# Performance work log

Hardware: AMD Instinct MI355X
Metric: run time of the kernel (lower is better)

## Reference

```python
import jax, jax.numpy as jnp
import numpy as np

SEQ_LEN, USER_LEN = 20, 256
INPUT_SIZE = 100000
NUM_CENTROIDS = 64
CAND = 1024
HIDDEN_DIM = 128
TOPK = 10
RHO = 0.02


def setup_inputs() -> dict:
    key = jax.random.key(0)
    ks = jax.random.split(key, 20)
    s = 0.1  # modest weight scale
    return {
        "x": jax.random.randint(ks[0], (SEQ_LEN, USER_LEN), 0, INPUT_SIZE),
        "t_slot": jax.random.randint(ks[1], (SEQ_LEN, USER_LEN), 0, 168),
        "vecs_use": jax.random.normal(ks[2], (INPUT_SIZE, 20), jnp.float32),
        "x_embedding_network": jax.random.normal(ks[3], (INPUT_SIZE, HIDDEN_DIM), jnp.float32),
        "I_array": jax.random.randint(ks[4], (INPUT_SIZE,), 0, NUM_CENTROIDS),
        "cand": jax.random.randint(ks[5], (NUM_CENTROIDS, CAND), 0, INPUT_SIZE),
        "time_embeddings": jax.random.normal(ks[6], (4, 20), jnp.float32),
        "W_seq1": jax.random.normal(ks[7], (100, 40), jnp.float32) * s,
        "b_seq1": jnp.zeros((40,), jnp.float32),
        "W_seq2": jax.random.normal(ks[8], (40, 20), jnp.float32) * s,
        "b_seq2": jnp.zeros((20,), jnp.float32),
        "W_to1": jax.random.normal(ks[9], (40, 40), jnp.float32) * s,
        "b_to1": jnp.zeros((40,), jnp.float32),
        "W_to2": jax.random.normal(ks[10], (40, 20), jnp.float32) * s,
        "b_to2": jnp.zeros((20,), jnp.float32),
        "W_ti1": jax.random.normal(ks[11], (40, 40), jnp.float32) * s,
        "b_ti1": jnp.zeros((40,), jnp.float32),
        "W_ti2": jax.random.normal(ks[12], (40, 20), jnp.float32) * s,
        "b_ti2": jnp.zeros((20,), jnp.float32),
    }


def _map_hour_to_segment(t):
    h = t % 24
    return jnp.where((h >= 22) | (h < 6), 0, jnp.where(h < 14, 1, 2))


def reference(x, t_slot, vecs_use, x_embedding_network, I_array, cand,
              time_embeddings, W_seq1, b_seq1, W_seq2, b_seq2,
              W_to1, b_to1, W_to2, b_to2, W_ti1, b_ti1, W_ti2, b_ti2):
    seq_len, user_len = x.shape
    x_view = x.reshape(-1)                                  # [N]
    x_emb = vecs_use[x_view].reshape(seq_len, user_len, 20)  # [S,U,20]

    # time-transfer (outgoing): concat(loc_emb, time_emb[segment]) -> MLP
    seg = _map_hour_to_segment(t_slot.reshape(-1))
    xc = jnp.concatenate([x_emb.reshape(-1, 20), time_embeddings[seg]], axis=-1)
    xi_out = jax.nn.relu(xc @ W_to1 + b_to1) @ W_to2 + b_to2  # [N,20]

    # candidate side: every location paired with fixed target segment 2
    seg2 = jnp.broadcast_to(time_embeddings[2], (vecs_use.shape[0], 20))
    vo = jnp.concatenate([vecs_use, seg2], axis=-1)
    vec_output = jax.nn.relu(vo @ W_ti1 + b_ti1) @ W_ti2 + b_ti2  # [V,20]

    # 5-step history (shift-with-edge-repeat) concat -> seq MLP
    def shift(k):
        return jnp.concatenate([x_emb[:k], x_emb[:seq_len - k]], axis=0)
    hist = jnp.concatenate(
        [shift(4), shift(3), shift(2), shift(1), x_emb], axis=-1).reshape(-1, 100)
    hist = jax.nn.relu(hist @ W_seq1 + b_seq1) @ W_seq2 + b_seq2  # [N,20]

    # per-token cluster routing + candidate distances
    a = 0.5 * (hist + xi_out)            # [N,20]
    c_idx = I_array[x_view]              # [N] cluster of each token's location
    cand_tok = cand[c_idx]               # [N,C] candidate loc ids
    Vg = vec_output[cand_tok]            # [N,C,20]
    d2 = (jnp.sum(a * a, -1)[:, None] + jnp.sum(Vg * Vg, -1)
          - 2.0 * jnp.einsum('nd,ncd->nc', a, Vg))
    dist = jnp.sqrt(jnp.maximum(d2, 1e-12))
    score = jnp.exp(-RHO * dist)         # [N,C]

    values, idx = jax.lax.top_k(score, TOPK)                 # [N,K]
    neigh_ids = jnp.take_along_axis(cand_tok, idx, axis=1)   # [N,K]
    emb_neigh = x_embedding_network[neigh_ids]               # [N,K,H]
    self_emb = x_embedding_network[x_view][:, None, :]       # [N,1,H]
    emb_all = jnp.concatenate([emb_neigh, self_emb], axis=1)  # [N,K+1,H]
    vals = jnp.concatenate(
        [values, jnp.ones((values.shape[0], 1), values.dtype)], axis=-1)
    w = jax.nn.softmax(vals, axis=-1)                        # [N,K+1]
    return jnp.sum(emb_all * w[..., None], axis=1)           # [N,H]
```

## Files before the change

### kernel.cpp

```cpp
#include <hip/hip_runtime.h>
#include <hip/hip_bf16.h>

#define SEQ_LEN   20
#define USER_LEN  256
#define NTOK      (SEQ_LEN * USER_LEN)
#define NC        64
#define CAND_N    1024
#define HID       128
#define TOPK      10
#define RHO_C     0.02f

#define CAND_BLKS (NC * CAND_N / 32)
#define TOK_BLKS  (NTOK / 16)
#define MAXB      (NTOK / 8 + NC)

__global__ __launch_bounds__(256) void k_pre(
    const int* __restrict__ x, const int* __restrict__ t_slot,
    const float* __restrict__ vecs, const float* __restrict__ temb,
    const int* __restrict__ I_array, const int* __restrict__ cand,
    const float* __restrict__ Ws1, const float* __restrict__ bs1,
    const float* __restrict__ Ws2, const float* __restrict__ bs2,
    const float* __restrict__ Wt1, const float* __restrict__ bt1,
    const float* __restrict__ Wt2, const float* __restrict__ bt2,
    const float* __restrict__ Wc1, const float* __restrict__ bc1,
    const float* __restrict__ Wc2, const float* __restrict__ bc2,
    float* __restrict__ tab, float* __restrict__ aArr, float* __restrict__ aNorm,
    int* __restrict__ bucket, int* __restrict__ blkInfo) {
  __shared__ union {
    struct { float sIn[32][20]; float sHid[32][40]; float sOut[32][21]; float sT[20]; } cd;
    struct { float sIn[16][140]; float sHid[16][80]; } tk;
    struct { int lc[NC]; int lcur[NC]; } kb;
  } U;
  int tid = threadIdx.x;

  if (blockIdx.x < CAND_BLKS) {
    int cc = tid >> 3, t = tid & 7;
    int g = blockIdx.x * 32 + cc;
    int v = cand[g];
    if (tid < 20) U.cd.sT[tid] = temb[40 + tid];
    for (int i = t; i < 20; i += 8) U.cd.sIn[cc][i] = vecs[(size_t)v * 20 + i];
    __syncthreads();

    #pragma unroll
    for (int q = 0; q < 5; q++) {
      int uu = t + 8 * q;
      float acc = bc1[uu];
      #pragma unroll
      for (int i = 0; i < 20; i++) acc = fmaf(U.cd.sIn[cc][i], Wc1[i * 40 + uu], acc);
      #pragma unroll
      for (int i = 0; i < 20; i++) acc = fmaf(U.cd.sT[i], Wc1[(20 + i) * 40 + uu], acc);
      U.cd.sHid[cc][uu] = fmaxf(acc, 0.f);
    }
    __syncthreads();

    #pragma unroll
    for (int rr = 0; rr < 3; rr++) {
      int o = t + 8 * rr;
      if (o < 20) {
        float acc = bc2[o];
        #pragma unroll
        for (int i = 0; i < 40; i++) acc = fmaf(U.cd.sHid[cc][i], Wc2[i * 20 + o], acc);
        U.cd.sOut[cc][o] = acc;
      }
    }
    __syncthreads();
    if (t == 0) {
      float nrm = 0.f;
      #pragma unroll
      for (int o = 0; o < 20; o++) nrm = fmaf(U.cd.sOut[cc][o], U.cd.sOut[cc][o], nrm);
      U.cd.sOut[cc][20] = nrm;
    }
    __syncthreads();

    int c = blockIdx.x >> 5;
    int jBase = (blockIdx.x & 31) * 32;
    float* base = tab + (size_t)c * (21 * CAND_N) + jBase;
    for (int idx = tid; idx < 21 * 32; idx += 256) {
      int o = idx >> 5, jj = idx & 31;
      base[o * CAND_N + jj] = U.cd.sOut[jj][o];
    }

  } else if (blockIdx.x < CAND_BLKS + TOK_BLKS) {
    int tt = tid >> 4, t = tid & 15;
    int n = (blockIdx.x - CAND_BLKS) * 16 + tt;
    int s = n >> 8, u = n & 255;
    int xv = x[n];
    int ts = t_slot[n];
    int h24 = ts % 24;
    int seg = (h24 >= 22 || h24 < 6) ? 0 : (h24 < 14 ? 1 : 2);

    for (int i = t; i < 140; i += 16) {
      float val;
      if (i < 20) val = vecs[(size_t)xv * 20 + i];
      else if (i < 40) val = temb[seg * 20 + (i - 20)];
      else {
        int ii = i - 40;
        int b = ii / 20, d = ii - b * 20;
        int sh = 4 - b;
        int row = (s >= sh) ? s - sh : s;
        int xv2 = (sh == 0) ? xv : x[row * USER_LEN + u];
        val = vecs[(size_t)xv2 * 20 + d];
      }
      U.tk.sIn[tt][i] = val;
    }
    __syncthreads();

    #pragma unroll
    for (int q = 0; q < 5; q++) {
      int uu = t + 16 * q;
      float acc;
      if (uu < 40) {
        acc = bt1[uu];
        #pragma unroll
        for (int i = 0; i < 40; i++) acc = fmaf(U.tk.sIn[tt][i], Wt1[i * 40 + uu], acc);
      } else {
        int u2 = uu - 40;
        acc = bs1[u2];
        #pragma unroll 4
        for (int i = 0; i < 100; i++) acc = fmaf(U.tk.sIn[tt][40 + i], Ws1[i * 40 + u2], acc);
      }
      U.tk.sHid[tt][uu] = fmaxf(acc, 0.f);
    }
    __syncthreads();

    #pragma unroll
    for (int rr = 0; rr < 2; rr++) {
      int o = t + 16 * rr;
      if (o < 20) {
        float acc = bt2[o] + bs2[o];
        #pragma unroll
        for (int i = 0; i < 40; i++) {
          acc = fmaf(U.tk.sHid[tt][i],      Wt2[i * 20 + o], acc);
          acc = fmaf(U.tk.sHid[tt][40 + i], Ws2[i * 20 + o], acc);
        }
        float av = 0.5f * acc;
        aArr[n * 20 + o] = av;
        U.tk.sIn[tt][o] = av;
      }
    }
    __syncthreads();
    if (t == 0) {
      float nrm = 0.f;
      #pragma unroll
      for (int o = 0; o < 20; o++) nrm = fmaf(U.tk.sIn[tt][o], U.tk.sIn[tt][o], nrm);
      aNorm[n] = nrm;
    }

  } else {
    if (tid < NC) U.kb.lc[tid] = 0;
    for (int b = tid; b < MAXB; b += 256) blkInfo[b] = -1;
    __syncthreads();
    for (int n = tid; n < NTOK; n += 256)
      atomicAdd(&U.kb.lc[I_array[x[n]]], 1);
    __syncthreads();

    int v = 0, myStart = 0, nb = 0, blkStart = 0;
    if (tid < 64) {
      v = U.kb.lc[tid];
      int inc = v;
      #pragma unroll
      for (int d = 1; d < 64; d <<= 1) {
        int t2 = __shfl_up(inc, d);
        if (tid >= d) inc += t2;
      }
      myStart = inc - v;
      U.kb.lcur[tid] = myStart;
      nb = (v + 7) >> 3;
      int nbs = nb;
      #pragma unroll
      for (int d = 1; d < 64; d <<= 1) {
        int t2 = __shfl_up(nbs, d);
        if (tid >= d) nbs += t2;
      }
      blkStart = nbs - nb;
    }
    __syncthreads();
    for (int n = tid; n < NTOK; n += 256) {
      int c = I_array[x[n]];
      int p = atomicAdd(&U.kb.lcur[c], 1);
      bucket[p] = n;
    }
    if (tid < 64) {
      for (int k = 0; k < nb; k++) {
        int rem = v - 8 * k;
        int tc = rem < 8 ? rem : 8;
        blkInfo[blkStart + k] = (tid << 20) | (tc << 16) | (myStart + 8 * k);
      }
    }
  }
}

__global__ __launch_bounds__(256) void k_distsel(
    const int* __restrict__ blkInfo, const int* __restrict__ bucket,
    const float* __restrict__ tab, const float* __restrict__ aArr,
    const float* __restrict__ aNorm, const int* __restrict__ x,
    const int* __restrict__ cand, const float* __restrict__ emb,
    float* __restrict__ out) {
  int info = blkInfo[blockIdx.x];
  if (info < 0) return;
  int start = info & 0xFFFF;
  int tcnt  = (info >> 16) & 0xF;
  int c     = info >> 20;

  __shared__ float sA[8][20];
  __shared__ float sN[8];
  __shared__ int   sTok[8];
  __shared__ float sD[8][CAND_N];

  int tid = threadIdx.x;
  if (tid < 8) {
    int live = tid < tcnt;
    int n = live ? bucket[start + tid] : 0;
    sTok[tid] = live ? n : -1;
    sN[tid] = live ? aNorm[n] : 0.f;
  }
  if (tid < 160) {
    int tt = tid / 20, d = tid - tt * 20;
    sA[tt][d] = (tt < tcnt) ? aArr[bucket[start + tt] * 20 + d] : 0.f;
  }
  __syncthreads();

  const float* T = tab + (size_t)c * (21 * CAND_N);
  int j4 = tid * 4;
  float4 acc[8];
  #pragma unroll
  for (int tt = 0; tt < 8; tt++) acc[tt] = make_float4(0.f, 0.f, 0.f, 0.f);
  #pragma unroll
  for (int dq = 0; dq < 5; dq++) {
    float4 t0 = *(const float4*)(T + (dq * 4 + 0) * CAND_N + j4);
    float4 t1 = *(const float4*)(T + (dq * 4 + 1) * CAND_N + j4);
    float4 t2 = *(const float4*)(T + (dq * 4 + 2) * CAND_N + j4);
    float4 t3 = *(const float4*)(T + (dq * 4 + 3) * CAND_N + j4);
    #pragma unroll
    for (int tt = 0; tt < 8; tt++) {
      float4 av = *(const float4*)(&sA[tt][dq * 4]);
      acc[tt].x = fmaf(av.x, t0.x, acc[tt].x);
      acc[tt].y = fmaf(av.x, t0.y, acc[tt].y);
      acc[tt].z = fmaf(av.x, t0.z, acc[tt].z);
      acc[tt].w = fmaf(av.x, t0.w, acc[tt].w);
      acc[tt].x = fmaf(av.y, t1.x, acc[tt].x);
      acc[tt].y = fmaf(av.y, t1.y, acc[tt].y);
      acc[tt].z = fmaf(av.y, t1.z, acc[tt].z);
      acc[tt].w = fmaf(av.y, t1.w, acc[tt].w);
      acc[tt].x = fmaf(av.z, t2.x, acc[tt].x);
      acc[tt].y = fmaf(av.z, t2.y, acc[tt].y);
      acc[tt].z = fmaf(av.z, t2.z, acc[tt].z);
      acc[tt].w = fmaf(av.z, t2.w, acc[tt].w);
      acc[tt].x = fmaf(av.w, t3.x, acc[tt].x);
      acc[tt].y = fmaf(av.w, t3.y, acc[tt].y);
      acc[tt].z = fmaf(av.w, t3.z, acc[tt].z);
      acc[tt].w = fmaf(av.w, t3.w, acc[tt].w);
    }
  }
  float4 cn4 = *(const float4*)(T + 20 * CAND_N + j4);
  #pragma unroll
  for (int tt = 0; tt < 8; tt++) {
    float4 d2;
    d2.x = sN[tt] + cn4.x - 2.f * acc[tt].x;
    d2.y = sN[tt] + cn4.y - 2.f * acc[tt].y;
    d2.z = sN[tt] + cn4.z - 2.f * acc[tt].z;
    d2.w = sN[tt] + cn4.w - 2.f * acc[tt].w;
    *(float4*)(&sD[tt][j4]) = d2;
  }
  __syncthreads();

  int lane = tid & 63, w = tid >> 6;
  #pragma unroll 1
  for (int pass = 0; pass < 2; pass++) {
    int tt = w + 4 * pass;
    if (tt >= tcnt) continue;
    int n = sTok[tt];
    int xv = x[n];

    float v[16];
    #pragma unroll
    for (int m = 0; m < 16; m++) v[m] = sD[tt][m * 64 + lane];

    float acc0 = 0.f, acc1 = 0.f, esum = 0.f;
    #pragma unroll 1
    for (int r = 0; r < TOPK; r++) {
      float bv = v[0];
      int bj = lane;
      #pragma unroll
      for (int m = 1; m < 16; m++) {
        int jm = (m << 6) | lane;
        if (v[m] < bv) { bv = v[m]; bj = jm; }
      }
      #pragma unroll
      for (int o = 1; o < 64; o <<= 1) {
        float ov = __shfl_xor(bv, o);
        int   oj = __shfl_xor(bj, o);
        if (ov < bv || (ov == bv && oj < bj)) { bv = ov; bj = oj; }
      }
      float dist = sqrtf(fmaxf(bv, 1e-12f));
      float e = expf(expf(-RHO_C * dist));
      int id = cand[c * CAND_N + bj];
      esum += e;
      acc0 = fmaf(e, emb[(size_t)id * HID + lane], acc0);
      acc1 = fmaf(e, emb[(size_t)id * HID + 64 + lane], acc1);
      #pragma unroll
      for (int m = 0; m < 16; m++) {
        int jm = (m << 6) | lane;
        if (jm == bj) v[m] = 3.0e38f;
      }
    }
    const float e1 = 2.71828182845904523536f;
    esum += e1;
    acc0 = fmaf(e1, emb[(size_t)xv * HID + lane], acc0);
    acc1 = fmaf(e1, emb[(size_t)xv * HID + 64 + lane], acc1);
    float inv = 1.0f / esum;
    out[(size_t)n * HID + lane] = acc0 * inv;
    out[(size_t)n * HID + 64 + lane] = acc1 * inv;
  }
}

extern "C" void kernel_launch(void* const* d_in, const int* in_sizes, int n_in,
                              void* d_out, int out_size, void* d_ws, size_t ws_size,
                              hipStream_t stream) {
  const int*   x      = (const int*)d_in[0];
  const int*   t_slot = (const int*)d_in[1];
  const float* vecs   = (const float*)d_in[2];
  const float* embn   = (const float*)d_in[3];
  const int*   I_arr  = (const int*)d_in[4];
  const int*   cand   = (const int*)d_in[5];
  const float* temb   = (const float*)d_in[6];
  const float* Ws1    = (const float*)d_in[7];
  const float* bs1    = (const float*)d_in[8];
  const float* Ws2    = (const float*)d_in[9];
  const float* bs2    = (const float*)d_in[10];
  const float* Wto1   = (const float*)d_in[11];
  const float* bto1   = (const float*)d_in[12];
  const float* Wto2   = (const float*)d_in[13];
  const float* bto2   = (const float*)d_in[14];
  const float* Wti1   = (const float*)d_in[15];
  const float* bti1   = (const float*)d_in[16];
  const float* Wti2   = (const float*)d_in[17];
  const float* bti2   = (const float*)d_in[18];

  float* tab    = (float*)d_ws;
  float* aArr   = tab + NC * 21 * CAND_N;
  float* aNorm  = aArr + NTOK * 20;
  int*   bucket = (int*)(aNorm + NTOK);
  int*   blkInfo= bucket + NTOK;
  float* outp   = (float*)d_out;

  k_pre<<<CAND_BLKS + TOK_BLKS + 1, 256, 0, stream>>>(
      x, t_slot, vecs, temb, I_arr, cand,
      Ws1, bs1, Ws2, bs2, Wto1, bto1, Wto2, bto2,
      Wti1, bti1, Wti2, bti2,
      tab, aArr, aNorm, bucket, blkInfo);
  k_distsel<<<MAXB, 256, 0, stream>>>(blkInfo, bucket, tab, aArr, aNorm,
                                      x, cand, embn, outp);
}
```

Measured before the change: 212.4 us.

## Map one item per thread in precompute MLPs and split token MLP branches

Measured after the change: 193.8 us. 8.8% less time.

```diff
diff --git a/kernel.cpp b/kernel.cpp
--- a/kernel.cpp
+++ b/kernel.cpp
@@ -10,11 +10,12 @@
 #define TOPK      10
 #define RHO_C     0.02f
 
-#define CAND_BLKS (NC * CAND_N / 32)
-#define TOK_BLKS  (NTOK / 16)
+#define CAND_BLKS 256
+#define TO_BLKS   (NTOK / 256)
+#define SEQ_BLKS  (NTOK / 256)
 #define MAXB      (NTOK / 8 + NC)
 
-__global__ __launch_bounds__(256) void k_pre(
+__global__ __launch_bounds__(256, 2) void k_pre(
     const int* __restrict__ x, const int* __restrict__ t_slot,
     const float* __restrict__ vecs, const float* __restrict__ temb,
     const int* __restrict__ I_array, const int* __restrict__ cand,
@@ -24,139 +25,147 @@
     const float* __restrict__ Wt2, const float* __restrict__ bt2,
     const float* __restrict__ Wc1, const float* __restrict__ bc1,
     const float* __restrict__ Wc2, const float* __restrict__ bc2,
-    float* __restrict__ tab, float* __restrict__ aArr, float* __restrict__ aNorm,
+    float* __restrict__ tab, float* __restrict__ aX, float* __restrict__ aH,
     int* __restrict__ bucket, int* __restrict__ blkInfo) {
-  __shared__ union {
-    struct { float sIn[32][20]; float sHid[32][40]; float sOut[32][21]; float sT[20]; } cd;
-    struct { float sIn[16][140]; float sHid[16][80]; } tk;
-    struct { int lc[NC]; int lcur[NC]; } kb;
-  } U;
   int tid = threadIdx.x;
 
   if (blockIdx.x < CAND_BLKS) {
-    int cc = tid >> 3, t = tid & 7;
-    int g = blockIdx.x * 32 + cc;
+    int g = blockIdx.x * 256 + tid;
     int v = cand[g];
-    if (tid < 20) U.cd.sT[tid] = temb[40 + tid];
-    for (int i = t; i < 20; i += 8) U.cd.sIn[cc][i] = vecs[(size_t)v * 20 + i];
-    __syncthreads();
-
+    float h[40];
+    #pragma unroll
+    for (int j = 0; j < 40; j++) h[j] = bc1[j];
     #pragma unroll
     for (int q = 0; q < 5; q++) {
-      int uu = t + 8 * q;
-      float acc = bc1[uu];
-      #pragma unroll
-      for (int i = 0; i < 20; i++) acc = fmaf(U.cd.sIn[cc][i], Wc1[i * 40 + uu], acc);
-      #pragma unroll
-      for (int i = 0; i < 20; i++) acc = fmaf(U.cd.sT[i], Wc1[(20 + i) * 40 + uu], acc);
-      U.cd.sHid[cc][uu] = fmaxf(acc, 0.f);
-    }
-    __syncthreads();
-
-    #pragma unroll
-    for (int rr = 0; rr < 3; rr++) {
-      int o = t + 8 * rr;
-      if (o < 20) {
-        float acc = bc2[o];
-        #pragma unroll
-        for (int i = 0; i < 40; i++) acc = fmaf(U.cd.sHid[cc][i], Wc2[i * 20 + o], acc);
-        U.cd.sOut[cc][o] = acc;
-      }
-    }
-    __syncthreads();
-    if (t == 0) {
-      float nrm = 0.f;
-      #pragma unroll
-      for (int o = 0; o < 20; o++) nrm = fmaf(U.cd.sOut[cc][o], U.cd.sOut[cc][o], nrm);
-      U.cd.sOut[cc][20] = nrm;
-    }
-    __syncthreads();
-
-    int c = blockIdx.x >> 5;
-    int jBase = (blockIdx.x & 31) * 32;
-    float* base = tab + (size_t)c * (21 * CAND_N) + jBase;
-    for (int idx = tid; idx < 21 * 32; idx += 256) {
-      int o = idx >> 5, jj = idx & 31;
-      base[o * CAND_N + jj] = U.cd.sOut[jj][o];
-    }
-
-  } else if (blockIdx.x < CAND_BLKS + TOK_BLKS) {
-    int tt = tid >> 4, t = tid & 15;
-    int n = (blockIdx.x - CAND_BLKS) * 16 + tt;
-    int s = n >> 8, u = n & 255;
+      float4 t4 = *(const float4*)(temb + 40 + 4 * q);
+      #pragma unroll
+      for (int r = 0; r < 4; r++) {
+        float ti = (&t4.x)[r];
+        #pragma unroll
+        for (int j = 0; j < 40; j++) h[j] = fmaf(ti, Wc1[(20 + 4 * q + r) * 40 + j], h[j]);
+      }
+    }
+    const float4* vp = (const float4*)(vecs + (size_t)v * 20);
+    #pragma unroll
+    for (int q = 0; q < 5; q++) {
+      float4 e = vp[q];
+      #pragma unroll
+      for (int r = 0; r < 4; r++) {
+        float xi = (&e.x)[r];
+        #pragma unroll
+        for (int j = 0; j < 40; j++) h[j] = fmaf(xi, Wc1[(4 * q + r) * 40 + j], h[j]);
+      }
+    }
+    float o[20];
+    #pragma unroll
+    for (int k = 0; k < 20; k++) o[k] = bc2[k];
+    #pragma unroll 8
+    for (int i = 0; i < 40; i++) {
+      float hv = fmaxf(h[i], 0.f);
+      #pragma unroll
+      for (int k = 0; k < 20; k++) o[k] = fmaf(hv, Wc2[i * 20 + k], o[k]);
+    }
+    int c = g >> 10, j = g & 1023;
+    float* op = tab + (size_t)c * (21 * CAND_N) + j;
+    float nrm = 0.f;
+    #pragma unroll
+    for (int k = 0; k < 20; k++) {
+      op[k * CAND_N] = o[k];
+      nrm = fmaf(o[k], o[k], nrm);
+    }
+    op[20 * CAND_N] = nrm;
+
+  } else if (blockIdx.x < CAND_BLKS + TO_BLKS) {
+    int n = (blockIdx.x - CAND_BLKS) * 256 + tid;
     int xv = x[n];
     int ts = t_slot[n];
     int h24 = ts % 24;
     int seg = (h24 >= 22 || h24 < 6) ? 0 : (h24 < 14 ? 1 : 2);
-
-    for (int i = t; i < 140; i += 16) {
-      float val;
-      if (i < 20) val = vecs[(size_t)xv * 20 + i];
-      else if (i < 40) val = temb[seg * 20 + (i - 20)];
-      else {
-        int ii = i - 40;
-        int b = ii / 20, d = ii - b * 20;
-        int sh = 4 - b;
-        int row = (s >= sh) ? s - sh : s;
-        int xv2 = (sh == 0) ? xv : x[row * USER_LEN + u];
-        val = vecs[(size_t)xv2 * 20 + d];
-      }
-      U.tk.sIn[tt][i] = val;
-    }
-    __syncthreads();
-
+    float h[40];
+    #pragma unroll
+    for (int j = 0; j < 40; j++) h[j] = bt1[j];
+    const float4* ep = (const float4*)(vecs + (size_t)xv * 20);
     #pragma unroll
     for (int q = 0; q < 5; q++) {
-      int uu = t + 16 * q;
-      float acc;
-      if (uu < 40) {
-        acc = bt1[uu];
-        #pragma unroll
-        for (int i = 0; i < 40; i++) acc = fmaf(U.tk.sIn[tt][i], Wt1[i * 40 + uu], acc);
-      } else {
-        int u2 = uu - 40;
-        acc = bs1[u2];
-        #pragma unroll 4
-        for (int i = 0; i < 100; i++) acc = fmaf(U.tk.sIn[tt][40 + i], Ws1[i * 40 + u2], acc);
-      }
-      U.tk.sHid[tt][uu] = fmaxf(acc, 0.f);
-    }
-    __syncthreads();
-
-    #pragma unroll
-    for (int rr = 0; rr < 2; rr++) {
-      int o = t + 16 * rr;
-      if (o < 20) {
-        float acc = bt2[o] + bs2[o];
-        #pragma unroll
-        for (int i = 0; i < 40; i++) {
-          acc = fmaf(U.tk.sHid[tt][i],      Wt2[i * 20 + o], acc);
-          acc = fmaf(U.tk.sHid[tt][40 + i], Ws2[i * 20 + o], acc);
+      float4 e = ep[q];
+      #pragma unroll
+      for (int r = 0; r < 4; r++) {
+        float xi = (&e.x)[r];
+        #pragma unroll
+        for (int j = 0; j < 40; j++) h[j] = fmaf(xi, Wt1[(4 * q + r) * 40 + j], h[j]);
+      }
+    }
+    const float4* tp = (const float4*)(temb + seg * 20);
+    #pragma unroll
+    for (int q = 0; q < 5; q++) {
+      float4 e = tp[q];
+      #pragma unroll
+      for (int r = 0; r < 4; r++) {
+        float xi = (&e.x)[r];
+        #pragma unroll
+        for (int j = 0; j < 40; j++) h[j] = fmaf(xi, Wt1[(20 + 4 * q + r) * 40 + j], h[j]);
+      }
+    }
+    float o[20];
+    #pragma unroll
+    for (int k = 0; k < 20; k++) o[k] = bt2[k];
+    #pragma unroll 8
+    for (int i = 0; i < 40; i++) {
+      float hv = fmaxf(h[i], 0.f);
+      #pragma unroll
+      for (int k = 0; k < 20; k++) o[k] = fmaf(hv, Wt2[i * 20 + k], o[k]);
+    }
+    #pragma unroll
+    for (int k = 0; k < 20; k++) aX[n * 20 + k] = o[k];
+
+  } else if (blockIdx.x < CAND_BLKS + TO_BLKS + SEQ_BLKS) {
+    int n = (blockIdx.x - CAND_BLKS - TO_BLKS) * 256 + tid;
+    int s = n >> 8, u = n & 255;
+    float h[40];
+    #pragma unroll
+    for (int j = 0; j < 40; j++) h[j] = bs1[j];
+    #pragma unroll 1
+    for (int b = 0; b < 5; b++) {
+      int sh = 4 - b;
+      int row = (s >= sh) ? s - sh : s;
+      int xv2 = x[row * USER_LEN + u];
+      const float4* p = (const float4*)(vecs + (size_t)xv2 * 20);
+      #pragma unroll
+      for (int q = 0; q < 5; q++) {
+        float4 e = p[q];
+        #pragma unroll
+        for (int r = 0; r < 4; r++) {
+          float xi = (&e.x)[r];
+          #pragma unroll
+          for (int j = 0; j < 40; j++) h[j] = fmaf(xi, Ws1[(b * 20 + 4 * q + r) * 40 + j], h[j]);
         }
-        float av = 0.5f * acc;
-        aArr[n * 20 + o] = av;
-        U.tk.sIn[tt][o] = av;
-      }
-    }
-    __syncthreads();
-    if (t == 0) {
-      float nrm = 0.f;
-      #pragma unroll
-      for (int o = 0; o < 20; o++) nrm = fmaf(U.tk.sIn[tt][o], U.tk.sIn[tt][o], nrm);
-      aNorm[n] = nrm;
-    }
+      }
+    }
+    float o[20];
+    #pragma unroll
+    for (int k = 0; k < 20; k++) o[k] = bs2[k];
+    #pragma unroll 8
+    for (int i = 0; i < 40; i++) {
+      float hv = fmaxf(h[i], 0.f);
+      #pragma unroll
+      for (int k = 0; k < 20; k++) o[k] = fmaf(hv, Ws2[i * 20 + k], o[k]);
+    }
+    #pragma unroll
+    for (int k = 0; k < 20; k++) aH[n * 20 + k] = o[k];
 
   } else {
-    if (tid < NC) U.kb.lc[tid] = 0;
+    __shared__ int lc[NC];
+    __shared__ int lcur[NC];
+    if (tid < NC) lc[tid] = 0;
     for (int b = tid; b < MAXB; b += 256) blkInfo[b] = -1;
     __syncthreads();
     for (int n = tid; n < NTOK; n += 256)
-      atomicAdd(&U.kb.lc[I_array[x[n]]], 1);
+      atomicAdd(&lc[I_array[x[n]]], 1);
     __syncthreads();
 
     int v = 0, myStart = 0, nb = 0, blkStart = 0;
     if (tid < 64) {
-      v = U.kb.lc[tid];
+      v = lc[tid];
       int inc = v;
       #pragma unroll
       for (int d = 1; d < 64; d <<= 1) {
@@ -164,7 +173,7 @@
         if (tid >= d) inc += t2;
       }
       myStart = inc - v;
-      U.kb.lcur[tid] = myStart;
+      lcur[tid] = myStart;
       nb = (v + 7) >> 3;
       int nbs = nb;
       #pragma unroll
@@ -177,7 +186,7 @@
     __syncthreads();
     for (int n = tid; n < NTOK; n += 256) {
       int c = I_array[x[n]];
-      int p = atomicAdd(&U.kb.lcur[c], 1);
+      int p = atomicAdd(&lcur[c], 1);
       bucket[p] = n;
     }
     if (tid < 64) {
@@ -192,8 +201,8 @@
 
 __global__ __launch_bounds__(256) void k_distsel(
     const int* __restrict__ blkInfo, const int* __restrict__ bucket,
-    const float* __restrict__ tab, const float* __restrict__ aArr,
-    const float* __restrict__ aNorm, const int* __restrict__ x,
+    const float* __restrict__ tab, const float* __restrict__ aX,
+    const float* __restrict__ aH, const int* __restrict__ x,
     const int* __restrict__ cand, const float* __restrict__ emb,
     float* __restrict__ out) {
   int info = blkInfo[blockIdx.x];
@@ -208,15 +217,22 @@
   __shared__ float sD[8][CAND_N];
 
   int tid = threadIdx.x;
-  if (tid < 8) {
-    int live = tid < tcnt;
-    int n = live ? bucket[start + tid] : 0;
-    sTok[tid] = live ? n : -1;
-    sN[tid] = live ? aNorm[n] : 0.f;
-  }
+  if (tid < 8) sTok[tid] = (tid < tcnt) ? bucket[start + tid] : -1;
   if (tid < 160) {
     int tt = tid / 20, d = tid - tt * 20;
-    sA[tt][d] = (tt < tcnt) ? aArr[bucket[start + tt] * 20 + d] : 0.f;
+    if (tt < tcnt) {
+      int n = bucket[start + tt];
+      sA[tt][d] = 0.5f * (aH[n * 20 + d] + aX[n * 20 + d]);
+    } else {
+      sA[tt][d] = 0.f;
+    }
+  }
+  __syncthreads();
+  if (tid < 8) {
+    float nrm = 0.f;
+    #pragma unroll
+    for (int d = 0; d < 20; d++) nrm = fmaf(sA[tid][d], sA[tid][d], nrm);
+    sN[tid] = nrm;
   }
   __syncthreads();
 
@@ -338,17 +354,17 @@
   const float* bti2   = (const float*)d_in[18];
 
   float* tab    = (float*)d_ws;
-  float* aArr   = tab + NC * 21 * CAND_N;
-  float* aNorm  = aArr + NTOK * 20;
-  int*   bucket = (int*)(aNorm + NTOK);
+  float* aX     = tab + NC * 21 * CAND_N;
+  float* aH     = aX + NTOK * 20;
+  int*   bucket = (int*)(aH + NTOK * 20);
   int*   blkInfo= bucket + NTOK;
   float* outp   = (float*)d_out;
 
-  k_pre<<<CAND_BLKS + TOK_BLKS + 1, 256, 0, stream>>>(
+  k_pre<<<CAND_BLKS + TO_BLKS + SEQ_BLKS + 1, 256, 0, stream>>>(
       x, t_slot, vecs, temb, I_arr, cand,
       Ws1, bs1, Ws2, bs2, Wto1, bto1, Wto2, bto2,
       Wti1, bti1, Wti2, bti2,
-      tab, aArr, aNorm, bucket, blkInfo);
-  k_distsel<<<MAXB, 256, 0, stream>>>(blkInfo, bucket, tab, aArr, aNorm,
+      tab, aX, aH, bucket, blkInfo);
+  k_distsel<<<MAXB, 256, 0, stream>>>(blkInfo, bucket, tab, aX, aH,
                                       x, cand, embn, outp);
 }
```
